# Optimization experiments

Hardware: AMD Instinct MI355X
Metric: run time of the kernel (lower is better)

## Reference

```python
import math
import jax, jax.numpy as jnp
import numpy as np

B, S, HID = 2, 2048, 2048
H, D = 32, 64  # num heads, head dim (H*D == HID)


def setup_inputs() -> dict:
    key = jax.random.key(0)
    ks = jax.random.split(key, 5)
    scale = 1.0 / math.sqrt(HID)
    return {
        "hidden_states": jax.random.normal(ks[0], (B, S, HID), dtype=jnp.float32),
        "attention_mask": jnp.zeros((B, S), dtype=jnp.float32),
        "wq": jax.random.normal(ks[1], (HID, HID), dtype=jnp.float32) * scale,
        "wk": jax.random.normal(ks[2], (HID, HID), dtype=jnp.float32) * scale,
        "wv": jax.random.normal(ks[3], (HID, HID), dtype=jnp.float32) * scale,
        "wo": jax.random.normal(ks[4], (HID, HID), dtype=jnp.float32) * scale,
    }


def reference(hidden_states, attention_mask, wq, wk, wv, wo):
    b, s, _ = hidden_states.shape
    # QKV projections (nn.Linear stores weight as [out, in]; y = x @ W^T)
    q = (hidden_states @ wq.T).reshape(b, s, H, D).transpose(0, 2, 1, 3)  # [B,H,S,D]
    k = (hidden_states @ wk.T).reshape(b, s, H, D).transpose(0, 2, 1, 3)
    v = (hidden_states @ wv.T).reshape(b, s, H, D).transpose(0, 2, 1, 3)
    # rotary_emb_ is None in the source module, so no RoPE is applied.
    scores = jnp.einsum("bhqd,bhkd->bhqk", q, k) / math.sqrt(D)  # [B,H,S,S]
    scores = scores + attention_mask.reshape(b, 1, 1, s)  # additive mask
    probs = jax.nn.softmax(scores, axis=-1)
    ctx = jnp.einsum("bhqk,bhkd->bhqd", probs, v)  # [B,H,S,D]
    ctx = ctx.transpose(0, 2, 1, 3).reshape(b, s, H * D)  # [B,S,HID]
    return ctx @ wo.T
```

## Files before the change

### kernel.cpp

```cpp
#include <hip/hip_runtime.h>

using bf16x8 = __attribute__((ext_vector_type(8))) __bf16;
using f32x4  = __attribute__((ext_vector_type(4))) float;
using uint2v = __attribute__((ext_vector_type(2))) unsigned int;

__device__ __forceinline__ unsigned short f2bf(float x) {
  unsigned int u = __float_as_uint(x);
  u += 0x7fffu + ((u >> 16) & 1u);
  return (unsigned short)(u >> 16);
}

__device__ __forceinline__ void gload16(const unsigned short* g, unsigned short* l) {
  __builtin_amdgcn_global_load_lds(
      (__attribute__((address_space(1))) void*)const_cast<unsigned short*>(g),
      (__attribute__((address_space(3))) void*)l, 16, 0, 0);
}

__global__ __launch_bounds__(256) void cvt_kernel(const float* __restrict__ in,
                                                  unsigned short* __restrict__ out) {
  const int i = blockIdx.x * 256 + threadIdx.x;
  const float4 v = ((const float4*)in)[i];
  ushort4 o;
  o.x = f2bf(v.x); o.y = f2bf(v.y); o.z = f2bf(v.z); o.w = f2bf(v.w);
  ((ushort4*)out)[i] = o;
}

template<int MODE>
__global__ __launch_bounds__(256)
void gemm_nt(const unsigned short* __restrict__ A,
             const unsigned short* __restrict__ Bw,
             float* __restrict__ Cf,
             unsigned short* __restrict__ Cq,
             int M, int N, int K)
{
  __shared__ unsigned short As[128 * 32];
  __shared__ unsigned short Bs[128 * 32];
  const int tid  = threadIdx.x;
  const int lane = tid & 63;
  const int wid  = tid >> 6;
  const int wr = wid >> 1, wc = wid & 1;
  const int lrow = lane & 15, lhi = lane >> 4;
  const int bn = blockIdx.x * 128;
  const int bm = blockIdx.y * 128;

  f32x4 acc[4][4] = {};

  const int srow = tid >> 2;
  const int scol = (tid & 3) * 8;
  const unsigned short* Ag0 = A  + (size_t)(bm + srow) * K + scol;
  const unsigned short* Ag1 = Ag0 + (size_t)64 * K;
  const unsigned short* Bg0 = Bw + (size_t)(bn + srow) * K + scol;
  const unsigned short* Bg1 = Bg0 + (size_t)64 * K;
  unsigned short* Ad0 = As + tid * 8;
  unsigned short* Ad1 = As + (256 + tid) * 8;
  unsigned short* Bd0 = Bs + tid * 8;
  unsigned short* Bd1 = Bs + (256 + tid) * 8;

  for (int k0 = 0; k0 < K; k0 += 32) {
    gload16(Ag0 + k0, Ad0);
    gload16(Ag1 + k0, Ad1);
    gload16(Bg0 + k0, Bd0);
    gload16(Bg1 + k0, Bd1);
    __syncthreads();
    bf16x8 af[4], bfr[4];
#pragma unroll
    for (int m = 0; m < 4; ++m)
      af[m] = *(const bf16x8*)(As + (wr * 64 + m * 16 + lrow) * 32 + lhi * 8);
#pragma unroll
    for (int n = 0; n < 4; ++n)
      bfr[n] = *(const bf16x8*)(Bs + (wc * 64 + n * 16 + lrow) * 32 + lhi * 8);
#pragma unroll
    for (int m = 0; m < 4; ++m)
#pragma unroll
      for (int n = 0; n < 4; ++n)
        acc[m][n] = __builtin_amdgcn_mfma_f32_16x16x32_bf16(af[m], bfr[n], acc[m][n], 0, 0, 0);
    __syncthreads();
  }

#pragma unroll
  for (int m = 0; m < 4; ++m) {
    const int row0 = bm + wr * 64 + m * 16 + lhi * 4;
#pragma unroll
    for (int n = 0; n < 4; ++n) {
      const int col = bn + wc * 64 + n * 16 + lrow;
#pragma unroll
      for (int r = 0; r < 4; ++r) {
        const int row = row0 + r;
        const float v = acc[m][n][r];
        if (MODE == 0) {
          const int which = col >> 11;
          const int h = (col >> 6) & 31;
          const int d = col & 63;
          const int b = row >> 11;
          const int s = row & 2047;
          if (which == 2) {
            Cq[(size_t)16777216 + ((size_t)(b * 32 + h) * 64 + d) * 2048 + s] = f2bf(v);
          } else {
            Cq[(((size_t)which * 64 + b * 32 + h) * 2048 + s) * 64 + d] = f2bf(v);
          }
        } else {
          Cf[(size_t)row * N + col] = v;
        }
      }
    }
  }
}

__global__ __launch_bounds__(256)
void attn_kernel(const unsigned short* __restrict__ QKV,
                 const float* __restrict__ mask,
                 unsigned short* __restrict__ Ctx)
{
  constexpr int S = 2048, D = 64, BH = 64;
  __shared__ unsigned short Klds[2][64 * 64];
  __shared__ unsigned short Vlds[2][64 * 64];
  __shared__ unsigned short PT[4][64 * 16];

  const int tid  = threadIdx.x;
  const int lane = tid & 63;
  const int wid  = tid >> 6;
  const int lrow = lane & 15;
  const int lhi  = lane >> 4;
  const int bh = blockIdx.y;
  const int b  = bh >> 5;
  const int h  = bh & 31;
  const int qbase = blockIdx.x * 64;

  const size_t qoff = (size_t)bh * S * D;
  const size_t koff = qoff + (size_t)BH * S * D;
  const size_t voff = koff + (size_t)BH * S * D;

  bf16x8 qa0, qa1;
  {
    const unsigned short* Qp = QKV + qoff + (size_t)(qbase + wid * 16 + lrow) * D + lhi * 8;
    qa0 = *(const bf16x8*)Qp;
    qa1 = *(const bf16x8*)(Qp + 32);
  }

  f32x4 oacc[4] = {};
  float srow[4] = {0.f, 0.f, 0.f, 0.f};

  const int strow  = tid >> 3;
  const int sswz   = ((tid & 7) ^ (strow & 7)) << 3;
  const unsigned short* Kg = QKV + koff + (size_t)strow * D + sswz;
  const unsigned short* Vg = QKV + voff + (size_t)strow * S + sswz;

  const float k1 = 0.125f * 1.44269504f;
  const unsigned ptbase =
      (unsigned)(uintptr_t)&PT[wid][0] + (unsigned)(lane * 8 + (lane >> 4) * 128);

  auto stage = [&](int t, int c) {
    const int kb = t * 64;
    gload16(Kg + (size_t)kb * D,          &Klds[c][0] + tid * 8);
    gload16(Kg + (size_t)kb * D + 32 * D, &Klds[c][0] + 2048 + tid * 8);
    gload16(Vg + kb,                      &Vlds[c][0] + tid * 8);
    gload16(Vg + kb + 32 * S,             &Vlds[c][0] + 2048 + tid * 8);
  };

  stage(0, 0);
  __syncthreads();

  for (int t = 0; t < S / 64; ++t) {
    const int kb  = t * 64;
    const int cur = t & 1;
    if (t + 1 < S / 64) stage(t + 1, cur ^ 1);

    float mkl[4];
#pragma unroll
    for (int f = 0; f < 4; ++f)
      mkl[f] = mask[(size_t)b * S + kb + lrow + 16 * f] * 1.44269504f;

    const unsigned short* Kc = &Klds[cur][0];
    f32x4 sacc[4] = {};
#pragma unroll
    for (int f = 0; f < 4; ++f) {
      const int krw = f * 16 + lrow;
      bf16x8 kf0 = *(const bf16x8*)(Kc + krw * 64 + ((lhi ^ (lrow & 7)) << 3));
      bf16x8 kf1 = *(const bf16x8*)(Kc + krw * 64 + (((lhi + 4) ^ (lrow & 7)) << 3));
      sacc[f] = __builtin_amdgcn_mfma_f32_16x16x32_bf16(qa0, kf0, sacc[f], 0, 0, 0);
      sacc[f] = __builtin_amdgcn_mfma_f32_16x16x32_bf16(qa1, kf1, sacc[f], 0, 0, 0);
    }

#pragma unroll
    for (int f = 0; f < 4; ++f)
#pragma unroll
      for (int r = 0; r < 4; ++r) {
        const float p = __builtin_amdgcn_exp2f(sacc[f][r] * k1 + mkl[f]);
        sacc[f][r] = p;
        srow[r] += p;
      }

    unsigned short* PTw = &PT[wid][0];
#pragma unroll
    for (int f = 0; f < 4; ++f) {
      unsigned w0, w1;
      asm("v_cvt_pk_bf16_f32 %0, %1, %2" : "=v"(w0) : "v"(sacc[f][0]), "v"(sacc[f][1]));
      asm("v_cvt_pk_bf16_f32 %0, %1, %2" : "=v"(w1) : "v"(sacc[f][2]), "v"(sacc[f][3]));
      uint2v w; w.x = w0; w.y = w1;
      *(uint2v*)(PTw + (lrow + 16 * f) * 16 + lhi * 4) = w;
    }

    const unsigned short* Vc = &Vlds[cur][0];
    uint2v r0, r1, r2, r3;
    asm volatile("ds_read_b64_tr_b16 %0, %1"             : "=v"(r0) : "v"(ptbase) : "memory");
    asm volatile("ds_read_b64_tr_b16 %0, %1 offset:128"  : "=v"(r1) : "v"(ptbase) : "memory");
    asm volatile("ds_read_b64_tr_b16 %0, %1 offset:1024" : "=v"(r2) : "v"(ptbase) : "memory");
    asm volatile("ds_read_b64_tr_b16 %0, %1 offset:1152" : "=v"(r3) : "v"(ptbase) : "memory");
    bf16x8 vb[2][4];
#pragma unroll
    for (int ks = 0; ks < 2; ++ks)
#pragma unroll
      for (int f = 0; f < 4; ++f) {
        const int dc = lrow + 16 * f;
        vb[ks][f] = *(const bf16x8*)(Vc + dc * 64 + (((ks * 4 + lhi) ^ (dc & 7)) << 3));
      }
    asm volatile("s_waitcnt lgkmcnt(0)" ::: "memory");
    __builtin_amdgcn_sched_barrier(0);
    union { struct { uint2v a, b; } u; bf16x8 v; } p0, p1;
    p0.u.a = r0; p0.u.b = r1;
    p1.u.a = r2; p1.u.b = r3;
#pragma unroll
    for (int f = 0; f < 4; ++f)
      oacc[f] = __builtin_amdgcn_mfma_f32_16x16x32_bf16(p0.v, vb[0][f], oacc[f], 0, 0, 0);
#pragma unroll
    for (int f = 0; f < 4; ++f)
      oacc[f] = __builtin_amdgcn_mfma_f32_16x16x32_bf16(p1.v, vb[1][f], oacc[f], 0, 0, 0);
    __syncthreads();
  }

#pragma unroll
  for (int off = 1; off < 16; off <<= 1)
#pragma unroll
    for (int r = 0; r < 4; ++r)
      srow[r] += __shfl_xor(srow[r], off, 64);

#pragma unroll
  for (int f = 0; f < 4; ++f) {
    const int d = lrow + 16 * f;
#pragma unroll
    for (int r = 0; r < 4; ++r) {
      const int q = qbase + wid * 16 + lhi * 4 + r;
      const float v = oacc[f][r] / srow[r];
      Ctx[((size_t)b * S + q) * 2048 + h * 64 + d] = f2bf(v);
    }
  }
}

extern "C" void kernel_launch(void* const* d_in, const int* in_sizes, int n_in,
                              void* d_out, int out_size, void* d_ws, size_t ws_size,
                              hipStream_t stream) {
  const float* X    = (const float*)d_in[0];
  const float* mask = (const float*)d_in[1];
  const float* wq   = (const float*)d_in[2];
  const float* wk   = (const float*)d_in[3];
  const float* wv   = (const float*)d_in[4];
  const float* wo   = (const float*)d_in[5];

  unsigned short* ws   = (unsigned short*)d_ws;
  unsigned short* Xb   = ws;
  unsigned short* Wcat = Xb + 8388608;
  unsigned short* Wob  = Wcat + 12582912;
  unsigned short* QKVb = Wob + 4194304;
  unsigned short* Ctxb = QKVb + 25165824;

  cvt_kernel<<<8192, 256, 0, stream>>>(X, Xb);
  cvt_kernel<<<4096, 256, 0, stream>>>(wq, Wcat);
  cvt_kernel<<<4096, 256, 0, stream>>>(wk, Wcat + 4194304);
  cvt_kernel<<<4096, 256, 0, stream>>>(wv, Wcat + 8388608);
  cvt_kernel<<<4096, 256, 0, stream>>>(wo, Wob);

  gemm_nt<0><<<dim3(48, 32), 256, 0, stream>>>(Xb, Wcat, nullptr, QKVb, 4096, 6144, 2048);

  attn_kernel<<<dim3(32, 64), 256, 0, stream>>>(QKVb, mask, Ctxb);

  gemm_nt<1><<<dim3(16, 32), 256, 0, stream>>>(Ctxb, Wob, (float*)d_out, nullptr, 4096, 2048, 2048);
}
```

Baseline: 498.4 us.

## Rewrite projection GEMMs with triple-buffered LDS pipeline and larger swizzled tiles

Replaces the simple single-buffer bf16 GEMM with a 512-thread kernel that uses 128x256 tiles and BK=64. Global-to-LDS loads run through a three-stage ring buffer so the next tiles load while MFMA runs. The kernel also adds an XOR swizzle on LDS columns to avoid bank conflicts, an XCD-aware block remap, and s_setprio around the MFMA loop. The cost is about 144KB of LDS and one block per CU, which lowers occupancy, and the out-projection grid shrinks to 256 blocks.

After: 456.2 us. 1.09x faster.

```diff
diff --git a/kernel.cpp b/kernel.cpp
--- a/kernel.cpp
+++ b/kernel.cpp
@@ -26,63 +26,101 @@
 }
 
 template<int MODE>
-__global__ __launch_bounds__(256)
-void gemm_nt(const unsigned short* __restrict__ A,
-             const unsigned short* __restrict__ Bw,
-             float* __restrict__ Cf,
-             unsigned short* __restrict__ Cq,
-             int M, int N, int K)
+__global__ __launch_bounds__(512, 1)
+void gemm3(const unsigned short* __restrict__ A,
+           const unsigned short* __restrict__ Bw,
+           float* __restrict__ Cf,
+           unsigned short* __restrict__ Cq,
+           int M, int N, int K)
 {
-  __shared__ unsigned short As[128 * 32];
-  __shared__ unsigned short Bs[128 * 32];
+  __shared__ unsigned short Sh[3 * 24576];
   const int tid  = threadIdx.x;
   const int lane = tid & 63;
   const int wid  = tid >> 6;
-  const int wr = wid >> 1, wc = wid & 1;
+  const int wm   = wid >> 2;
+  const int wn   = wid & 3;
   const int lrow = lane & 15, lhi = lane >> 4;
-  const int bn = blockIdx.x * 128;
-  const int bm = blockIdx.y * 128;
+
+  const int gY   = gridDim.y;
+  const int nwg  = gridDim.x * gY;
+  const int flat = blockIdx.x * gY + blockIdx.y;
+  const int swzb = (flat & 7) * (nwg >> 3) + (flat >> 3);
+  const int bn   = (swzb / gY) * 256;
+  const int bm   = (swzb % gY) * 128;
+
+  const int NT = K >> 6;
+
+  const int srow = tid >> 3;
+  const int sswz = (((tid & 7) ^ (srow & 7)) << 3);
+  const unsigned short* AgS = A  + (size_t)(bm + srow) * K + sswz;
+  const unsigned short* BgS = Bw + (size_t)(bn + srow) * K + sswz;
+
+  auto stage = [&](int t, unsigned short* base) {
+    const unsigned short* ag = AgS + (size_t)t * 64;
+    const unsigned short* bg = BgS + (size_t)t * 64;
+    gload16(ag,                   base + tid * 8);
+    gload16(ag + (size_t)64 * K,  base + 4096  + tid * 8);
+    gload16(bg,                   base + 8192  + tid * 8);
+    gload16(bg + (size_t)64 * K,  base + 12288 + tid * 8);
+    gload16(bg + (size_t)128 * K, base + 16384 + tid * 8);
+    gload16(bg + (size_t)192 * K, base + 20480 + tid * 8);
+  };
+
+  int aoff[4], boff[4], coff[2];
+#pragma unroll
+  for (int m = 0; m < 4; ++m) aoff[m] = (wm * 64 + m * 16 + lrow) * 64;
+#pragma unroll
+  for (int n = 0; n < 4; ++n) boff[n] = 8192 + (wn * 64 + n * 16 + lrow) * 64;
+  coff[0] = ((lhi)     ^ (lrow & 7)) << 3;
+  coff[1] = ((lhi + 4) ^ (lrow & 7)) << 3;
 
   f32x4 acc[4][4] = {};
 
-  const int srow = tid >> 2;
-  const int scol = (tid & 3) * 8;
-  const unsigned short* Ag0 = A  + (size_t)(bm + srow) * K + scol;
-  const unsigned short* Ag1 = Ag0 + (size_t)64 * K;
-  const unsigned short* Bg0 = Bw + (size_t)(bn + srow) * K + scol;
-  const unsigned short* Bg1 = Bg0 + (size_t)64 * K;
-  unsigned short* Ad0 = As + tid * 8;
-  unsigned short* Ad1 = As + (256 + tid) * 8;
-  unsigned short* Bd0 = Bs + tid * 8;
-  unsigned short* Bd1 = Bs + (256 + tid) * 8;
-
-  for (int k0 = 0; k0 < K; k0 += 32) {
-    gload16(Ag0 + k0, Ad0);
-    gload16(Ag1 + k0, Ad1);
-    gload16(Bg0 + k0, Bd0);
-    gload16(Bg1 + k0, Bd1);
-    __syncthreads();
-    bf16x8 af[4], bfr[4];
-#pragma unroll
-    for (int m = 0; m < 4; ++m)
-      af[m] = *(const bf16x8*)(As + (wr * 64 + m * 16 + lrow) * 32 + lhi * 8);
-#pragma unroll
-    for (int n = 0; n < 4; ++n)
-      bfr[n] = *(const bf16x8*)(Bs + (wc * 64 + n * 16 + lrow) * 32 + lhi * 8);
-#pragma unroll
-    for (int m = 0; m < 4; ++m)
-#pragma unroll
-      for (int n = 0; n < 4; ++n)
-        acc[m][n] = __builtin_amdgcn_mfma_f32_16x16x32_bf16(af[m], bfr[n], acc[m][n], 0, 0, 0);
-    __syncthreads();
+  stage(0, Sh);
+  stage(1, Sh + 24576);
+  asm volatile("s_waitcnt vmcnt(6)" ::: "memory");
+  __builtin_amdgcn_s_barrier();
+
+  int cb = 0;
+  for (int t = 0; t < NT; ++t) {
+    if (t + 2 < NT) {
+      int sb = cb + 2; if (sb >= 3) sb -= 3;
+      stage(t + 2, Sh + sb * 24576);
+    }
+    const unsigned short* crd = Sh + cb * 24576;
+    bf16x8 a_[2][4], b_[2][4];
+#pragma unroll
+    for (int ks = 0; ks < 2; ++ks) {
+#pragma unroll
+      for (int m = 0; m < 4; ++m) a_[ks][m] = *(const bf16x8*)(crd + aoff[m] + coff[ks]);
+#pragma unroll
+      for (int n = 0; n < 4; ++n) b_[ks][n] = *(const bf16x8*)(crd + boff[n] + coff[ks]);
+    }
+    __builtin_amdgcn_s_setprio(1);
+#pragma unroll
+    for (int ks = 0; ks < 2; ++ks)
+#pragma unroll
+      for (int m = 0; m < 4; ++m)
+#pragma unroll
+        for (int n = 0; n < 4; ++n)
+          acc[m][n] = __builtin_amdgcn_mfma_f32_16x16x32_bf16(a_[ks][m], b_[ks][n], acc[m][n], 0, 0, 0);
+    __builtin_amdgcn_s_setprio(0);
+    if (t + 2 < NT) {
+      asm volatile("s_waitcnt vmcnt(6)" ::: "memory");
+      __builtin_amdgcn_s_barrier();
+    } else if (t + 1 < NT) {
+      asm volatile("s_waitcnt vmcnt(0)" ::: "memory");
+      __builtin_amdgcn_s_barrier();
+    }
+    cb = (cb + 1 == 3) ? 0 : cb + 1;
   }
 
 #pragma unroll
   for (int m = 0; m < 4; ++m) {
-    const int row0 = bm + wr * 64 + m * 16 + lhi * 4;
+    const int row0 = bm + wm * 64 + m * 16 + lhi * 4;
 #pragma unroll
     for (int n = 0; n < 4; ++n) {
-      const int col = bn + wc * 64 + n * 16 + lrow;
+      const int col = bn + wn * 64 + n * 16 + lrow;
 #pragma unroll
       for (int r = 0; r < 4; ++r) {
         const int row = row0 + r;
@@ -269,9 +307,9 @@
   cvt_kernel<<<4096, 256, 0, stream>>>(wv, Wcat + 8388608);
   cvt_kernel<<<4096, 256, 0, stream>>>(wo, Wob);
 
-  gemm_nt<0><<<dim3(48, 32), 256, 0, stream>>>(Xb, Wcat, nullptr, QKVb, 4096, 6144, 2048);
+  gemm3<0><<<dim3(24, 32), 512, 0, stream>>>(Xb, Wcat, nullptr, QKVb, 4096, 6144, 2048);
 
   attn_kernel<<<dim3(32, 64), 256, 0, stream>>>(QKVb, mask, Ctxb);
 
-  gemm_nt<1><<<dim3(16, 32), 256, 0, stream>>>(Ctxb, Wob, (float*)d_out, nullptr, 4096, 2048, 2048);
-}
+  gemm3<1><<<dim3(8, 32), 512, 0, stream>>>(Ctxb, Wob, (float*)d_out, nullptr, 4096, 2048, 2048);
+}
```
